# Kernel tuning notes

Measured on AMD Instinct MI355X. Metric: run time of the kernel, lower is better.

Reference implementation:

```python
import jax, jax.numpy as jnp
import numpy as np

B = 65536
D = 512            # resnet18 fc.in_features
NUM_CLASSES = 512  # size of batch_centers
LEVELS = [2048, 1024, 512]


def setup_inputs() -> dict:
    key = jax.random.key(0)
    ks = jax.random.split(key, 8)
    x = jax.random.normal(ks[0], (B, D), dtype=jnp.float32)
    labels = jax.random.randint(ks[1], (B,), 0, NUM_CLASSES, dtype=jnp.int64)
    W0 = jax.random.normal(ks[2], (LEVELS[0], D), dtype=jnp.float32) * 0.02
    b0 = jnp.zeros((LEVELS[0],), dtype=jnp.float32)
    W1 = jax.random.normal(ks[3], (LEVELS[1], LEVELS[0]), dtype=jnp.float32) * 0.02
    b1 = jnp.zeros((LEVELS[1],), dtype=jnp.float32)
    W2 = jax.random.normal(ks[4], (LEVELS[2], LEVELS[1]), dtype=jnp.float32) * 0.02
    b2 = jnp.zeros((LEVELS[2],), dtype=jnp.float32)
    lambda_values = jnp.array([1e-3, 1.0, 1.0, 1.0], dtype=jnp.float32)
    return {"x": x, "W0": W0, "b0": b0, "W1": W1, "b1": b1,
            "W2": W2, "b2": b2, "lambda_values": lambda_values,
            "labels": labels}


def _cross_entropy(logits, labels):
    # mean over batch of -log p(label) (torch CrossEntropyLoss default)
    logp = jax.nn.log_softmax(logits, axis=-1)
    nll = -jnp.take_along_axis(logp, labels[:, None], axis=-1)[:, 0]
    return jnp.mean(nll)


def reference(x, W0, b0, W1, b1, W2, b2, lambda_values, labels):
    # --- per-class scatter-mean centers (vectorized segment reduce) ---
    sums = jax.ops.segment_sum(x, labels, num_segments=NUM_CLASSES)
    counts = jax.ops.segment_sum(jnp.ones((x.shape[0],), x.dtype), labels,
                                 num_segments=NUM_CLASSES)
    centers = jnp.where(counts[:, None] > 0,
                        sums / jnp.maximum(counts, 1.0)[:, None],
                        0.0)  # classes absent from batch keep zero centers
    # --- gather-diff center loss: sum_i ||x_i - c_{y_i}||^2 ---
    diff = x - centers[labels]
    center_loss = jnp.sum(diff * diff)
    # --- cascaded classification heads, CE at each level ---
    h = x
    losses = []
    for W, b in ((W0, b0), (W1, b1), (W2, b2)):
        h = h @ W.T + b
        losses.append(_cross_entropy(h, labels))
    classification_losses = jnp.stack(losses)
    return lambda_values[0] * center_loss + jnp.dot(lambda_values[1:],
                                                    classification_losses)
```

## Files before the change

kernel.cpp:

```cpp
#include <hip/hip_runtime.h>
#include <cstdint>
#include <cstddef>

using f32x4  = __attribute__((ext_vector_type(4))) float;
using i32x4v = __attribute__((ext_vector_type(4))) int;
using i32x8v = __attribute__((ext_vector_type(8))) int;

__device__ __forceinline__ unsigned char f2fp8(float f) {
  return (unsigned char)(__builtin_amdgcn_cvt_pk_fp8_f32(f, f, 0, false) & 0xff);
}

__device__ __forceinline__ float fp8b0(unsigned int w) {
  return __builtin_amdgcn_cvt_f32_fp8(w, 0);
}
__device__ __forceinline__ float fp8b1(unsigned int w) {
  return __builtin_amdgcn_cvt_f32_fp8(w, 1);
}
__device__ __forceinline__ float fp8b2(unsigned int w) {
  return __builtin_amdgcn_cvt_f32_fp8(w, 2);
}
__device__ __forceinline__ float fp8b3(unsigned int w) {
  return __builtin_amdgcn_cvt_f32_fp8(w, 3);
}

__device__ __forceinline__ float waveRed(float v) {
#pragma unroll
  for (int m = 32; m >= 1; m >>= 1) v += __shfl_xor(v, m, 64);
  return v;
}

__device__ __forceinline__ void gload16(const void* g, void* l) {
  __builtin_amdgcn_global_load_lds(
      (__attribute__((address_space(1))) uint32_t*)(uintptr_t)g,
      (__attribute__((address_space(3))) uint32_t*)(uint32_t*)l,
      16, 0, 0);
}

__device__ __forceinline__ i32x8v cvt32(const float* p) {
  const float4* p4 = (const float4*)p;
  int d0, d1, d2, d3, d4, d5, d6, d7;
#define CVT1(N)                                                      \
  {                                                                  \
    const float4 f = p4[N];                                          \
    int w_ = __builtin_amdgcn_cvt_pk_fp8_f32(f.x, f.y, 0, false);    \
    w_ = __builtin_amdgcn_cvt_pk_fp8_f32(f.z, f.w, w_, true);        \
    d##N = w_;                                                       \
  }
  CVT1(0) CVT1(1) CVT1(2) CVT1(3) CVT1(4) CVT1(5) CVT1(6) CVT1(7)
#undef CVT1
  return (i32x8v){d0, d1, d2, d3, d4, d5, d6, d7};
}

__device__ __forceinline__ i32x8v ldfrag(const unsigned char* bb, int off) {
  const i32x4v lo = *(const i32x4v*)(bb + off);
  const i32x4v hi = *(const i32x4v*)(bb + off + 1024);
  return (i32x8v){lo[0], lo[1], lo[2], lo[3], hi[0], hi[1], hi[2], hi[3]};
}

__global__ __launch_bounds__(256) void prep_w(
    const float4* __restrict__ W1, const float4* __restrict__ W2,
    const float4* __restrict__ W0f4, const float* __restrict__ W0,
    const float* __restrict__ b0,
    uint32_t* __restrict__ W1_8, uint32_t* __restrict__ W2_8,
    uint32_t* __restrict__ W0_8, unsigned char* __restrict__ W0t8,
    float* __restrict__ zr, int zwords, float* __restrict__ biascat) {
  __shared__ unsigned char t8[64][65];
  const int b = blockIdx.x;
  const int tid = threadIdx.x;
  if (b < 1024) {
    for (int i = b * 256 + tid; i < 524288; i += 1024 * 256) {
      float4 v = W1[i];
      int p = __builtin_amdgcn_cvt_pk_fp8_f32(v.x, v.y, 0, false);
      p = __builtin_amdgcn_cvt_pk_fp8_f32(v.z, v.w, p, true);
      W1_8[i] = (uint32_t)p;
    }
  } else if (b < 1280) {
    for (int i = (b - 1024) * 256 + tid; i < 131072; i += 256 * 256) {
      float4 v = W2[i];
      int p = __builtin_amdgcn_cvt_pk_fp8_f32(v.x, v.y, 0, false);
      p = __builtin_amdgcn_cvt_pk_fp8_f32(v.z, v.w, p, true);
      W2_8[i] = (uint32_t)p;
    }
  } else if (b < 1536) {
    for (int i = (b - 1280) * 256 + tid; i < 262144; i += 256 * 256) {
      float4 v = W0f4[i];
      int p = __builtin_amdgcn_cvt_pk_fp8_f32(v.x, v.y, 0, false);
      p = __builtin_amdgcn_cvt_pk_fp8_f32(v.z, v.w, p, true);
      W0_8[i] = (uint32_t)p;
    }
  } else if (b < 1792) {
    const int t = b - 1536;
    const int r0 = (t >> 3) * 64, c0 = (t & 7) * 64;
#pragma unroll
    for (int p = 0; p < 16; ++p) {
      const int row = p * 4 + (tid >> 6), col = tid & 63;
      t8[row][col] = f2fp8(W0[(size_t)(r0 + row) * 512 + c0 + col]);
    }
    __syncthreads();
#pragma unroll
    for (int p = 0; p < 16; ++p) {
      const int oc = p * 4 + (tid >> 6), orr = tid & 63;
      W0t8[(size_t)(c0 + oc) * 2048 + r0 + orr] = t8[orr][oc];
    }
  } else {
    const int zb = (zwords + 255) >> 8;
    if (b < 1792 + zb) {
      const int i = (b - 1792) * 256 + tid;
      if (i < zwords) zr[i] = 0.f;
    } else {
      const int i = (b - 1792 - zb) * 256 + tid;
      if (i < 2048) biascat[i] = b0[i];
    }
  }
}

__global__ __launch_bounds__(256) void count_k(const int* __restrict__ lab,
                                               int* __restrict__ counts, int n) {
  __shared__ int h[512];
  for (int i = threadIdx.x; i < 512; i += 256) h[i] = 0;
  __syncthreads();
  for (int i = blockIdx.x * 256 + threadIdx.x; i < n; i += gridDim.x * 256)
    atomicAdd(&h[lab[i]], 1);
  __syncthreads();
  for (int i = threadIdx.x; i < 512; i += 256) {
    int v = h[i];
    if (v) atomicAdd(&counts[i], v);
  }
}

__global__ void prefix_k(const int* __restrict__ counts, int* __restrict__ offsets,
                         int* __restrict__ cursor, int nc) {
  const int lane = threadIdx.x;
  int base = 0;
  for (int c0 = 0; c0 < nc; c0 += 64) {
    int v = counts[c0 + lane];
    int x = v;
#pragma unroll
    for (int d = 1; d < 64; d <<= 1) {
      int y = __shfl_up(x, d, 64);
      if (lane >= d) x += y;
    }
    int excl = base + x - v;
    offsets[c0 + lane] = excl;
    cursor[c0 + lane] = excl;
    base += __shfl(x, 63, 64);
  }
}

__global__ void scatter_k(const int* __restrict__ lab, int* __restrict__ cursor,
                          int* __restrict__ buckets, int n) {
  for (int i = blockIdx.x * 256 + threadIdx.x; i < n; i += gridDim.x * 256) {
    int pos = atomicAdd(&cursor[lab[i]], 1);
    buckets[pos] = i;
  }
}

__global__ __launch_bounds__(256) void csum_k(const float* __restrict__ x,
    const int* __restrict__ buckets, const int* __restrict__ offsets,
    const int* __restrict__ counts, float* __restrict__ centers4,
    float* __restrict__ scal) {
  const int c = blockIdx.x >> 2, q = blockIdx.x & 3;
  const int cnt = counts[c];
  const int t = threadIdx.x;
  float sx = 0.f, sy = 0.f, ssq = 0.f;
  if (cnt) {
    const int beg = offsets[c];
    const int lo = beg + (cnt * q) / 4, hi = beg + (cnt * (q + 1)) / 4;
    for (int i = lo; i < hi; ++i) {
      const int row = buckets[i];
      const float2 v = ((const float2*)(x + (size_t)row * 512))[t];
      sx += v.x;
      sy += v.y;
      ssq += v.x * v.x + v.y * v.y;
    }
  }
  float2* dst = (float2*)(centers4 + (size_t)((c << 2) + q) * 512);
  dst[t] = make_float2(sx, sy);
  ssq = waveRed(ssq);
  __shared__ float red[4];
  if ((t & 63) == 0) red[t >> 6] = ssq;
  __syncthreads();
  if (t == 0) {
    const float s = red[0] + red[1] + red[2] + red[3];
    if (s != 0.f) atomicAdd(&scal[0], s);
  }
}

__global__ __launch_bounds__(256) void cnorm_k(const float* __restrict__ centers4,
    float* __restrict__ centers, const int* __restrict__ counts,
    float* __restrict__ out) {
  const int c = blockIdx.x;
  const int t = threadIdx.x;
  const float2* p = (const float2*)(centers4 + (size_t)(c << 2) * 512);
  float2 s = p[t];
  float2 s1 = p[t + 256], s2 = p[t + 512], s3 = p[t + 768];
  s.x += s1.x + s2.x + s3.x;
  s.y += s1.y + s2.y + s3.y;
  ((float2*)(centers + (size_t)c * 512))[t] = s;
  const int cnt = counts[c];
  if (cnt == 0) return;
  float ssq = s.x * s.x + s.y * s.y;
  ssq = waveRed(ssq);
  __shared__ float red[4];
  if ((t & 63) == 0) red[t >> 6] = ssq;
  __syncthreads();
  if (t == 0)
    atomicAdd(out, (red[0] + red[1] + red[2] + red[3]) / (float)cnt);
}

__global__ __launch_bounds__(256) void matvec_k(const float* __restrict__ W,
    const float* __restrict__ vin, const float* __restrict__ badd,
    float* __restrict__ vout, int K) {
  int row = blockIdx.x;
  float s = 0.f;
  for (int k = threadIdx.x; k < K; k += 256) s += W[(size_t)row * K + k] * vin[k];
  s = waveRed(s);
  __shared__ float red[4];
  if ((threadIdx.x & 63) == 0) red[threadIdx.x >> 6] = s;
  __syncthreads();
  if (threadIdx.x == 0) vout[row] = red[0] + red[1] + red[2] + red[3] + badd[row];
}

__global__ void pk_k(const float* __restrict__ centers,
                     const unsigned char* __restrict__ Bcat8,
                     const float* __restrict__ biascat,
                     const int* __restrict__ counts, float* __restrict__ scal) {
  const int b = blockIdx.x;
  const int lvl = b >> 9;
  const int c = b & 511;
  const int lane = threadIdx.x;
  const int cbase = (lvl == 0) ? 0 : (lvl == 1) ? 2048 : 3072;
  const float4* S = (const float4*)(centers + (size_t)c * 512);
  const uint2 wb = ((const uint2*)(Bcat8 + (size_t)(cbase + c) * 512))[lane];
  const float4 s0 = S[lane * 2];
  const float4 s1 = S[lane * 2 + 1];
  float s = s0.x * fp8b0(wb.x) + s0.y * fp8b1(wb.x) +
            s0.z * fp8b2(wb.x) + s0.w * fp8b3(wb.x) +
            s1.x * fp8b0(wb.y) + s1.y * fp8b1(wb.y) +
            s1.z * fp8b2(wb.y) + s1.w * fp8b3(wb.y);
  s = waveRed(s);
  if (lane == 0)
    atomicAdd(&scal[5 + lvl], s + (float)counts[c] * biascat[cbase + c]);
}

__global__ __launch_bounds__(256) void gemm8_w(
    const unsigned char* __restrict__ A8, const unsigned char* __restrict__ B8,
    int M, int N, int K, unsigned char* __restrict__ C8,
    unsigned char* __restrict__ Ct8) {
  __shared__ __align__(16) unsigned char As[128 * 128];
  __shared__ __align__(16) unsigned char Bs[128 * 128];
  const int tid = threadIdx.x;
  const int lane = tid & 63;
  const int wave = tid >> 6;
  const int lane16 = lane & 15;
  const int quad = lane >> 4;
  const int wm = (wave >> 1) * 64;
  const int wn = (wave & 1) * 64;
  const int m0 = blockIdx.y * 128;
  const int n0 = blockIdx.x * 128;

  f32x4 acc[4][4] = {};

  int srow[4], goff[4];
#pragma unroll
  for (int q = 0; q < 4; ++q) {
    const int s = tid + q * 256;
    const int row = s >> 3;
    const int c16 = s & 7;
    srow[q] = row;
    goff[q] = (((c16 >> 1) ^ (row & 3)) << 5) + ((c16 & 1) << 4);
  }

  for (int kt = 0; kt < K; kt += 128) {
#pragma unroll
    for (int q = 0; q < 4; ++q) {
      const int s = tid + q * 256;
      gload16(A8 + (size_t)(m0 + srow[q]) * K + kt + goff[q], &As[s * 16]);
      gload16(B8 + (size_t)(n0 + srow[q]) * K + kt + goff[q], &Bs[s * 16]);
    }
    __syncthreads();
    i32x8v a8[4], b8[4];
#pragma unroll
    for (int i = 0; i < 4; ++i) {
      const int row = i * 16 + lane16;
      const int sc = quad ^ (row & 3);
      const unsigned char* pa = &As[row * 128 + sc * 32];
      const i32x4v lo = *(const i32x4v*)pa;
      const i32x4v hi = *(const i32x4v*)(pa + 16);
      a8[i] = (i32x8v){lo[0], lo[1], lo[2], lo[3], hi[0], hi[1], hi[2], hi[3]};
    }
#pragma unroll
    for (int j = 0; j < 4; ++j) {
      const int row = j * 16 + lane16;
      const int sc = quad ^ (row & 3);
      const unsigned char* pb = &Bs[row * 128 + sc * 32];
      const i32x4v lo = *(const i32x4v*)pb;
      const i32x4v hi = *(const i32x4v*)(pb + 16);
      b8[j] = (i32x8v){lo[0], lo[1], lo[2], lo[3], hi[0], hi[1], hi[2], hi[3]};
    }
#pragma unroll
    for (int i = 0; i < 4; ++i)
#pragma unroll
      for (int j = 0; j < 4; ++j)
        acc[i][j] = __builtin_amdgcn_mfma_scale_f32_16x16x128_f8f6f4(
            a8[i], b8[j], acc[i][j], 0, 0, 0, 0x7f7f7f7f, 0, 0x7f7f7f7f);
    __syncthreads();
  }
#pragma unroll
  for (int i = 0; i < 4; ++i)
#pragma unroll
    for (int r = 0; r < 4; ++r) {
      const int rowg = m0 + wm + i * 16 + quad * 4 + r;
#pragma unroll
      for (int j = 0; j < 4; ++j) {
        const int colg = n0 + wn + j * 16 + lane16;
        const unsigned char v8 = f2fp8(acc[i][j][r]);
        C8[(size_t)rowg * N + colg] = v8;
        if (Ct8) Ct8[(size_t)colg * M + rowg] = v8;
      }
    }
}

__global__ void reorder_k(const unsigned char* __restrict__ in,
                          unsigned char* __restrict__ out) {
  const int id = blockIdx.x * 256 + threadIdx.x;
  const int col = id >> 4;
  const int k32 = id & 15;
  const int kt = k32 >> 2, quad = k32 & 3;
  const int l = quad * 16 + (col & 15);
  const size_t src = (size_t)col * 512 + k32 * 32;
  const size_t fragbase = (size_t)(col >> 6) * 32768 + (size_t)kt * 8192 +
                          (size_t)((col >> 4) & 3) * 2048;
  const uint4 a = *(const uint4*)(in + src);
  const uint4 b = *(const uint4*)(in + src + 16);
  *(uint4*)(out + fragbase + l * 16) = a;
  *(uint4*)(out + fragbase + 1024 + l * 16) = b;
}

__global__ __launch_bounds__(256, 2) void gemm_ce8(
    const float* __restrict__ x, const unsigned char* __restrict__ Bp,
    const float* __restrict__ bias, float* __restrict__ scal) {
  __shared__ __align__(16) unsigned char Bl[4][8192];
  __shared__ float biasl[3584];
  const int tid = threadIdx.x;
  const int lane = tid & 63;
  const int wave = tid >> 6;
  const int lane16 = lane & 15;
  const int quad = lane >> 4;
  const int m0 = blockIdx.x * 128 + wave * 32;

  for (int i = tid; i < 3584; i += 256) biasl[i] = bias[i];

  const float* xr0 = x + (size_t)(m0 + lane16) * 512 + quad * 32;
  const float* xr1 = x + (size_t)(m0 + 16 + lane16) * 512 + quad * 32;
  i32x8v a00 = cvt32(xr0);
  i32x8v a01 = cvt32(xr0 + 128);
  i32x8v a02 = cvt32(xr0 + 256);
  i32x8v a03 = cvt32(xr0 + 384);
  i32x8v a10 = cvt32(xr1);
  i32x8v a11 = cvt32(xr1 + 128);
  i32x8v a12 = cvt32(xr1 + 256);
  i32x8v a13 = cvt32(xr1 + 384);
  __syncthreads();

  const int soff = wave * 2048 + lane * 16;
  const unsigned char* bsrc = Bp + soff;
#pragma unroll
  for (int c = 0; c < 3; ++c) {
    gload16(bsrc, &Bl[c][soff]);
    gload16(bsrc + 1024, &Bl[c][soff + 1024]);
    bsrc += 8192;
  }
  int sc = 3;
  asm volatile("s_waitcnt vmcnt(4)" ::: "memory");
  __builtin_amdgcn_s_barrier();

  const int l16 = lane * 16;
  i32x8v bx0, bx1, bx2, bx3, by0, by1, by2, by3;
  {
    const unsigned char* bb = &Bl[0][0];
    bx0 = ldfrag(bb, l16);
    bx1 = ldfrag(bb, 2048 + l16);
    bx2 = ldfrag(bb, 4096 + l16);
    bx3 = ldfrag(bb, 6144 + l16);
  }

  float es[8];
#pragma unroll
  for (int k = 0; k < 8; ++k) es[k] = 0.f;

#define MFMA8(A0, A1, B0, B1, B2, B3)                                         \
  acc00 = __builtin_amdgcn_mfma_scale_f32_16x16x128_f8f6f4(                   \
      A0, B0, acc00, 0, 0, 0, 0x7f7f7f7f, 0, 0x7f7f7f7f);                     \
  acc01 = __builtin_amdgcn_mfma_scale_f32_16x16x128_f8f6f4(                   \
      A0, B1, acc01, 0, 0, 0, 0x7f7f7f7f, 0, 0x7f7f7f7f);                     \
  acc02 = __builtin_amdgcn_mfma_scale_f32_16x16x128_f8f6f4(                   \
      A0, B2, acc02, 0, 0, 0, 0x7f7f7f7f, 0, 0x7f7f7f7f);                     \
  acc03 = __builtin_amdgcn_mfma_scale_f32_16x16x128_f8f6f4(                   \
      A0, B3, acc03, 0, 0, 0, 0x7f7f7f7f, 0, 0x7f7f7f7f);                     \
  acc10 = __builtin_amdgcn_mfma_scale_f32_16x16x128_f8f6f4(                   \
      A1, B0, acc10, 0, 0, 0, 0x7f7f7f7f, 0, 0x7f7f7f7f);                     \
  acc11 = __builtin_amdgcn_mfma_scale_f32_16x16x128_f8f6f4(                   \
      A1, B1, acc11, 0, 0, 0, 0x7f7f7f7f, 0, 0x7f7f7f7f);                     \
  acc12 = __builtin_amdgcn_mfma_scale_f32_16x16x128_f8f6f4(                   \
      A1, B2, acc12, 0, 0, 0, 0x7f7f7f7f, 0, 0x7f7f7f7f);                     \
  acc13 = __builtin_amdgcn_mfma_scale_f32_16x16x128_f8f6f4(                   \
      A1, B3, acc13, 0, 0, 0, 0x7f7f7f7f, 0, 0x7f7f7f7f);

#define KSTEP(KS, BC0, BC1, BC2, BC3, BN0, BN1, BN2, BN3, A0, A1)             \
  {                                                                           \
    gload16(bsrc, &Bl[(KS + 3) & 3][soff]);                                   \
    gload16(bsrc + 1024, &Bl[(KS + 3) & 3][soff + 1024]);                     \
    bsrc += 8192;                                                             \
    if (++sc == 224) { sc = 0; bsrc = Bp + soff; }                            \
    asm volatile("s_waitcnt vmcnt(4)" ::: "memory");                          \
    __builtin_amdgcn_s_barrier();                                             \
    {                                                                         \
      const unsigned char* bb = &Bl[(KS + 1) & 3][0];                         \
      BN0 = ldfrag(bb, l16);                                                  \
      BN1 = ldfrag(bb, 2048 + l16);                                           \
      BN2 = ldfrag(bb, 4096 + l16);                                           \
      BN3 = ldfrag(bb, 6144 + l16);                                           \
    }                                                                         \
    asm volatile("s_waitcnt lgkmcnt(8)" ::: "memory");                        \
    __builtin_amdgcn_sched_barrier(0);                                        \
    __builtin_amdgcn_s_setprio(1);                                            \
    MFMA8(A0, A1, BC0, BC1, BC2, BC3)                                         \
    __builtin_amdgcn_s_setprio(0);                                            \
  }

  int tile = 0;
#pragma unroll 1
  for (int lvl = 0; lvl < 3; ++lvl) {
    const int nt = (lvl == 0) ? 32 : (lvl == 1) ? 16 : 8;
#pragma unroll 1
    for (int t = 0; t < nt; ++t, ++tile) {
      f32x4 acc00 = {}, acc01 = {}, acc02 = {}, acc03 = {};
      f32x4 acc10 = {}, acc11 = {}, acc12 = {}, acc13 = {};
      KSTEP(0, bx0, bx1, bx2, bx3, by0, by1, by2, by3, a00, a10)
      KSTEP(1, by0, by1, by2, by3, bx0, bx1, bx2, bx3, a01, a11)
      KSTEP(2, bx0, bx1, bx2, bx3, by0, by1, by2, by3, a02, a12)
      KSTEP(3, by0, by1, by2, by3, bx0, bx1, bx2, bx3, a03, a13)
      const float bj0 = biasl[tile * 64 + lane16];
      const float bj1 = biasl[tile * 64 + 16 + lane16];
      const float bj2 = biasl[tile * 64 + 32 + lane16];
      const float bj3 = biasl[tile * 64 + 48 + lane16];
#pragma unroll
      for (int r = 0; r < 4; ++r) {
        es[r] += __expf(acc00[r] + bj0) + __expf(acc01[r] + bj1) +
                 __expf(acc02[r] + bj2) + __expf(acc03[r] + bj3);
        es[4 + r] += __expf(acc10[r] + bj0) + __expf(acc11[r] + bj1) +
                     __expf(acc12[r] + bj2) + __expf(acc13[r] + bj3);
      }
    }
    float ls = 0.f;
#pragma unroll
    for (int k = 0; k < 8; ++k) {
      float tot = es[k];
      tot += __shfl_xor(tot, 1, 64);
      tot += __shfl_xor(tot, 2, 64);
      tot += __shfl_xor(tot, 4, 64);
      tot += __shfl_xor(tot, 8, 64);
      if (lane16 == 0) ls += __logf(tot);
      es[k] = 0.f;
    }
    ls = waveRed(ls);
    if (lane == 0) atomicAdd(&scal[2 + lvl], ls);
  }
#undef KSTEP
#undef MFMA8
}

__global__ void fin_k(const float* __restrict__ scal, const float* __restrict__ lam,
                      float* __restrict__ out, float invB) {
  if (threadIdx.x == 0 && blockIdx.x == 0)
    out[0] = lam[0] * (scal[0] - scal[1]) +
             (lam[1] * (scal[2] - scal[5]) + lam[2] * (scal[3] - scal[6]) +
              lam[3] * (scal[4] - scal[7])) * invB;
}

extern "C" void kernel_launch(void* const* d_in, const int* in_sizes, int n_in,
                              void* d_out, int out_size, void* d_ws, size_t ws_size,
                              hipStream_t stream) {
  const float* x   = (const float*)d_in[0];
  const float* W0  = (const float*)d_in[1];
  const float* b0  = (const float*)d_in[2];
  const float* W1  = (const float*)d_in[3];
  const float* b1  = (const float*)d_in[4];
  const float* W2  = (const float*)d_in[5];
  const float* b2  = (const float*)d_in[6];
  const float* lam = (const float*)d_in[7];
  const int*   lab = (const int*)d_in[8];

  const int Bsz = in_sizes[8];
  const int D   = in_sizes[0] / Bsz;
  const int N0  = in_sizes[2];
  const int N1  = in_sizes[4];
  const int N2  = in_sizes[6];
  const int Ncat = N0 + N1 + N2;
  const int NCLS = 512;

  char* w = (char*)d_ws;
  size_t off = 0;
  auto alloc = [&](size_t bytes) -> void* {
    void* p = w + off;
    off += (bytes + 255) & ~(size_t)255;
    return p;
  };

  unsigned char* Bcat8 = (unsigned char*)alloc((size_t)Ncat * D);
  unsigned char* Bp    = (unsigned char*)alloc((size_t)Ncat * D + 16384);
  unsigned char* W1_8  = (unsigned char*)alloc((size_t)N1 * N0);
  unsigned char* W2_8  = (unsigned char*)alloc((size_t)N2 * N1);
  unsigned char* W0t8  = (unsigned char*)alloc((size_t)D * N0);
  unsigned char* M1t8  = (unsigned char*)alloc((size_t)D * N1);
  float* biascat  = (float*)alloc((size_t)Ncat * 4);
  int* offsets = (int*)alloc(NCLS * 4);
  int* cursor  = (int*)alloc(NCLS * 4);
  int* buckets = (int*)alloc((size_t)Bsz * 4);
  float* centers4 = (float*)alloc((size_t)NCLS * 512 * 4 * 4);
  float* centers  = (float*)alloc((size_t)NCLS * 512 * 4);
  const int zwords = NCLS + 8;
  char* zr = (char*)alloc((size_t)zwords * 4);
  int*   counts  = (int*)zr;
  float* scal    = (float*)(zr + NCLS * 4);
  (void)ws_size; (void)n_in; (void)out_size;

  const int zb = (zwords + 255) / 256;
  prep_w<<<dim3(1792 + zb + 8), dim3(256), 0, stream>>>(
      (const float4*)W1, (const float4*)W2, (const float4*)W0, W0, b0,
      (uint32_t*)W1_8, (uint32_t*)W2_8, (uint32_t*)Bcat8, W0t8,
      (float*)zr, zwords, biascat);

  count_k<<<dim3(32), dim3(256), 0, stream>>>(lab, counts, Bsz);
  prefix_k<<<dim3(1), dim3(64), 0, stream>>>(counts, offsets, cursor, NCLS);
  scatter_k<<<dim3(256), dim3(256), 0, stream>>>(lab, cursor, buckets, Bsz);
  csum_k<<<dim3(4 * NCLS), dim3(256), 0, stream>>>(x, buckets, offsets, counts,
                                                   centers4, scal);
  cnorm_k<<<dim3(NCLS), dim3(256), 0, stream>>>(centers4, centers, counts,
                                                &scal[1]);

  matvec_k<<<dim3(N1), dim3(256), 0, stream>>>(W1, b0, b1, biascat + N0, N0);
  matvec_k<<<dim3(N2), dim3(256), 0, stream>>>(W2, biascat + N0, b2, biascat + N0 + N1, N1);

  gemm8_w<<<dim3(D / 128, N1 / 128), dim3(256), 0, stream>>>(
      W1_8, W0t8, N1, D, N0, Bcat8 + (size_t)N0 * D, M1t8);
  gemm8_w<<<dim3(D / 128, N2 / 128), dim3(256), 0, stream>>>(
      W2_8, M1t8, N2, D, N1, Bcat8 + (size_t)(N0 + N1) * D, nullptr);

  reorder_k<<<dim3(Ncat * D / 32 / 256), dim3(256), 0, stream>>>(Bcat8, Bp);

  pk_k<<<dim3(3 * NCLS), dim3(64), 0, stream>>>(centers, Bcat8, biascat,
                                                counts, scal);

  gemm_ce8<<<dim3(Bsz / 128), dim3(256), 0, stream>>>(x, Bp, biascat, scal);

  fin_k<<<dim3(1), dim3(64), 0, stream>>>(scal, lam, (float*)d_out, 1.f / (float)Bsz);
}
```

Measured before the change: 519.6 us.

## Double rows per wave in fused FP8 GEMM-CE and interleave B fragment loads

Each wave now covers 64 rows instead of 32, so every block handles 256 rows and each B tile staged in LDS feeds twice as many MFMAs. The grid is halved and launch bounds drop to one block per SM, which raises register use (16 accumulators, 16 A fragments). B fragments are now read from LDS one at a time and interleaved with groups of four MFMAs instead of being prefetched a whole k-step ahead. The aim is to cut LDS and global B traffic per FLOP, at the cost of lower occupancy and less latency hiding.

New measurement: 563.0 us. 8.4% more time.

```diff
diff --git a/kernel.cpp b/kernel.cpp
--- a/kernel.cpp
+++ b/kernel.cpp
@@ -337,7 +337,7 @@
   *(uint4*)(out + fragbase + 1024 + l * 16) = b;
 }
 
-__global__ __launch_bounds__(256, 2) void gemm_ce8(
+__global__ __launch_bounds__(256, 1) void gemm_ce8(
     const float* __restrict__ x, const unsigned char* __restrict__ Bp,
     const float* __restrict__ bias, float* __restrict__ scal) {
   __shared__ __align__(16) unsigned char Bl[4][8192];
@@ -347,20 +347,17 @@
   const int wave = tid >> 6;
   const int lane16 = lane & 15;
   const int quad = lane >> 4;
-  const int m0 = blockIdx.x * 128 + wave * 32;
+  const int m0 = blockIdx.x * 256 + wave * 64;
 
   for (int i = tid; i < 3584; i += 256) biasl[i] = bias[i];
 
-  const float* xr0 = x + (size_t)(m0 + lane16) * 512 + quad * 32;
-  const float* xr1 = x + (size_t)(m0 + 16 + lane16) * 512 + quad * 32;
-  i32x8v a00 = cvt32(xr0);
-  i32x8v a01 = cvt32(xr0 + 128);
-  i32x8v a02 = cvt32(xr0 + 256);
-  i32x8v a03 = cvt32(xr0 + 384);
-  i32x8v a10 = cvt32(xr1);
-  i32x8v a11 = cvt32(xr1 + 128);
-  i32x8v a12 = cvt32(xr1 + 256);
-  i32x8v a13 = cvt32(xr1 + 384);
+  i32x8v a[4][4];
+#pragma unroll
+  for (int i = 0; i < 4; ++i) {
+    const float* xr = x + (size_t)(m0 + i * 16 + lane16) * 512 + quad * 32;
+#pragma unroll
+    for (int kt = 0; kt < 4; ++kt) a[i][kt] = cvt32(xr + kt * 128);
+  }
   __syncthreads();
 
   const int soff = wave * 2048 + lane * 16;
@@ -376,57 +373,46 @@
   __builtin_amdgcn_s_barrier();
 
   const int l16 = lane * 16;
-  i32x8v bx0, bx1, bx2, bx3, by0, by1, by2, by3;
-  {
-    const unsigned char* bb = &Bl[0][0];
-    bx0 = ldfrag(bb, l16);
-    bx1 = ldfrag(bb, 2048 + l16);
-    bx2 = ldfrag(bb, 4096 + l16);
-    bx3 = ldfrag(bb, 6144 + l16);
-  }
-
-  float es[8];
-#pragma unroll
-  for (int k = 0; k < 8; ++k) es[k] = 0.f;
-
-#define MFMA8(A0, A1, B0, B1, B2, B3)                                         \
-  acc00 = __builtin_amdgcn_mfma_scale_f32_16x16x128_f8f6f4(                   \
-      A0, B0, acc00, 0, 0, 0, 0x7f7f7f7f, 0, 0x7f7f7f7f);                     \
-  acc01 = __builtin_amdgcn_mfma_scale_f32_16x16x128_f8f6f4(                   \
-      A0, B1, acc01, 0, 0, 0, 0x7f7f7f7f, 0, 0x7f7f7f7f);                     \
-  acc02 = __builtin_amdgcn_mfma_scale_f32_16x16x128_f8f6f4(                   \
-      A0, B2, acc02, 0, 0, 0, 0x7f7f7f7f, 0, 0x7f7f7f7f);                     \
-  acc03 = __builtin_amdgcn_mfma_scale_f32_16x16x128_f8f6f4(                   \
-      A0, B3, acc03, 0, 0, 0, 0x7f7f7f7f, 0, 0x7f7f7f7f);                     \
-  acc10 = __builtin_amdgcn_mfma_scale_f32_16x16x128_f8f6f4(                   \
-      A1, B0, acc10, 0, 0, 0, 0x7f7f7f7f, 0, 0x7f7f7f7f);                     \
-  acc11 = __builtin_amdgcn_mfma_scale_f32_16x16x128_f8f6f4(                   \
-      A1, B1, acc11, 0, 0, 0, 0x7f7f7f7f, 0, 0x7f7f7f7f);                     \
-  acc12 = __builtin_amdgcn_mfma_scale_f32_16x16x128_f8f6f4(                   \
-      A1, B2, acc12, 0, 0, 0, 0x7f7f7f7f, 0, 0x7f7f7f7f);                     \
-  acc13 = __builtin_amdgcn_mfma_scale_f32_16x16x128_f8f6f4(                   \
-      A1, B3, acc13, 0, 0, 0, 0x7f7f7f7f, 0, 0x7f7f7f7f);
-
-#define KSTEP(KS, BC0, BC1, BC2, BC3, BN0, BN1, BN2, BN3, A0, A1)             \
+  float es[16];
+#pragma unroll
+  for (int k = 0; k < 16; ++k) es[k] = 0.f;
+
+#define MFMA4(KS, BF, J)                                                      \
+  acc[0][J] = __builtin_amdgcn_mfma_scale_f32_16x16x128_f8f6f4(               \
+      a[0][KS], BF, acc[0][J], 0, 0, 0, 0x7f7f7f7f, 0, 0x7f7f7f7f);           \
+  acc[1][J] = __builtin_amdgcn_mfma_scale_f32_16x16x128_f8f6f4(               \
+      a[1][KS], BF, acc[1][J], 0, 0, 0, 0x7f7f7f7f, 0, 0x7f7f7f7f);           \
+  acc[2][J] = __builtin_amdgcn_mfma_scale_f32_16x16x128_f8f6f4(               \
+      a[2][KS], BF, acc[2][J], 0, 0, 0, 0x7f7f7f7f, 0, 0x7f7f7f7f);           \
+  acc[3][J] = __builtin_amdgcn_mfma_scale_f32_16x16x128_f8f6f4(               \
+      a[3][KS], BF, acc[3][J], 0, 0, 0, 0x7f7f7f7f, 0, 0x7f7f7f7f);
+
+#define KSTEP(KS)                                                             \
   {                                                                           \
     gload16(bsrc, &Bl[(KS + 3) & 3][soff]);                                   \
     gload16(bsrc + 1024, &Bl[(KS + 3) & 3][soff + 1024]);                     \
     bsrc += 8192;                                                             \
     if (++sc == 224) { sc = 0; bsrc = Bp + soff; }                            \
+    i32x8v bf0 = ldfrag(&Bl[KS][0], l16);                                     \
+    i32x8v bf1 = ldfrag(&Bl[KS][0], 2048 + l16);                              \
+    asm volatile("s_waitcnt lgkmcnt(2)" ::: "memory");                        \
+    __builtin_amdgcn_sched_barrier(0);                                        \
+    __builtin_amdgcn_s_setprio(1);                                            \
+    MFMA4(KS, bf0, 0)                                                         \
+    i32x8v bf2 = ldfrag(&Bl[KS][0], 4096 + l16);                              \
+    asm volatile("s_waitcnt lgkmcnt(2)" ::: "memory");                        \
+    __builtin_amdgcn_sched_barrier(0);                                        \
+    MFMA4(KS, bf1, 1)                                                         \
+    i32x8v bf3 = ldfrag(&Bl[KS][0], 6144 + l16);                              \
+    asm volatile("s_waitcnt lgkmcnt(2)" ::: "memory");                        \
+    __builtin_amdgcn_sched_barrier(0);                                        \
+    MFMA4(KS, bf2, 2)                                                         \
+    asm volatile("s_waitcnt lgkmcnt(0)" ::: "memory");                        \
+    __builtin_amdgcn_sched_barrier(0);                                        \
+    MFMA4(KS, bf3, 3)                                                         \
+    __builtin_amdgcn_s_setprio(0);                                            \
     asm volatile("s_waitcnt vmcnt(4)" ::: "memory");                          \
     __builtin_amdgcn_s_barrier();                                             \
-    {                                                                         \
-      const unsigned char* bb = &Bl[(KS + 1) & 3][0];                         \
-      BN0 = ldfrag(bb, l16);                                                  \
-      BN1 = ldfrag(bb, 2048 + l16);                                           \
-      BN2 = ldfrag(bb, 4096 + l16);                                           \
-      BN3 = ldfrag(bb, 6144 + l16);                                           \
-    }                                                                         \
-    asm volatile("s_waitcnt lgkmcnt(8)" ::: "memory");                        \
-    __builtin_amdgcn_sched_barrier(0);                                        \
-    __builtin_amdgcn_s_setprio(1);                                            \
-    MFMA8(A0, A1, BC0, BC1, BC2, BC3)                                         \
-    __builtin_amdgcn_s_setprio(0);                                            \
   }
 
   int tile = 0;
@@ -435,27 +421,27 @@
     const int nt = (lvl == 0) ? 32 : (lvl == 1) ? 16 : 8;
 #pragma unroll 1
     for (int t = 0; t < nt; ++t, ++tile) {
-      f32x4 acc00 = {}, acc01 = {}, acc02 = {}, acc03 = {};
-      f32x4 acc10 = {}, acc11 = {}, acc12 = {}, acc13 = {};
-      KSTEP(0, bx0, bx1, bx2, bx3, by0, by1, by2, by3, a00, a10)
-      KSTEP(1, by0, by1, by2, by3, bx0, bx1, bx2, bx3, a01, a11)
-      KSTEP(2, bx0, bx1, bx2, bx3, by0, by1, by2, by3, a02, a12)
-      KSTEP(3, by0, by1, by2, by3, bx0, bx1, bx2, bx3, a03, a13)
+      f32x4 acc[4][4] = {};
+      KSTEP(0)
+      KSTEP(1)
+      KSTEP(2)
+      KSTEP(3)
       const float bj0 = biasl[tile * 64 + lane16];
       const float bj1 = biasl[tile * 64 + 16 + lane16];
       const float bj2 = biasl[tile * 64 + 32 + lane16];
       const float bj3 = biasl[tile * 64 + 48 + lane16];
 #pragma unroll
-      for (int r = 0; r < 4; ++r) {
-        es[r] += __expf(acc00[r] + bj0) + __expf(acc01[r] + bj1) +
-                 __expf(acc02[r] + bj2) + __expf(acc03[r] + bj3);
-        es[4 + r] += __expf(acc10[r] + bj0) + __expf(acc11[r] + bj1) +
-                     __expf(acc12[r] + bj2) + __expf(acc13[r] + bj3);
-      }
+      for (int i = 0; i < 4; ++i)
+#pragma unroll
+        for (int r = 0; r < 4; ++r)
+          es[i * 4 + r] += __expf(acc[i][0][r] + bj0) +
+                           __expf(acc[i][1][r] + bj1) +
+                           __expf(acc[i][2][r] + bj2) +
+                           __expf(acc[i][3][r] + bj3);
     }
     float ls = 0.f;
 #pragma unroll
-    for (int k = 0; k < 8; ++k) {
+    for (int k = 0; k < 16; ++k) {
       float tot = es[k];
       tot += __shfl_xor(tot, 1, 64);
       tot += __shfl_xor(tot, 2, 64);
@@ -468,7 +454,7 @@
     if (lane == 0) atomicAdd(&scal[2 + lvl], ls);
   }
 #undef KSTEP
-#undef MFMA8
+#undef MFMA4
 }
 
 __global__ void fin_k(const float* __restrict__ scal, const float* __restrict__ lam,
@@ -553,7 +539,7 @@
   pk_k<<<dim3(3 * NCLS), dim3(64), 0, stream>>>(centers, Bcat8, biascat,
                                                 counts, scal);
 
-  gemm_ce8<<<dim3(Bsz / 128), dim3(256), 0, stream>>>(x, Bp, biascat, scal);
+  gemm_ce8<<<dim3(Bsz / 256), dim3(256), 0, stream>>>(x, Bp, biascat, scal);
 
   fin_k<<<dim3(1), dim3(64), 0, stream>>>(scal, lam, (float*)d_out, 1.f / (float)Bsz);
 }
```
